# Kernel tuning notes

Hardware: AMD Instinct MI355X
Metric: run time of the kernel (lower is better)

## Reference

```python
import jax, jax.numpy as jnp
import numpy as np

P2 = 8
BN_EPS = 1e-5


def _slice_maps(p2):
    # Faithfully reproduce the buggy fs[:, i*j-1] indexing: later loop
    # iterations overwrite earlier ones; slots never written stay zero.
    last = {}
    for i in range(1, p2 + 1):
        for j in range(1, p2 + 1):
            last[i * j - 1] = (i - 1, j - 1)
    src_i = np.zeros(p2 * p2, np.int32)
    src_j = np.zeros(p2 * p2, np.int32)
    mask = np.zeros(p2 * p2, np.float32)
    for k, (ii, jj) in last.items():
        src_i[k], src_j[k], mask[k] = ii, jj, 1.0
    # unslice: output patch (i,j) reads slot (i+1)*(j+1)-1
    uns = np.array([[(i + 1) * (j + 1) - 1 for j in range(p2)] for i in range(p2)], np.int32)
    return src_i, src_j, mask, uns


def setup_inputs() -> dict:
    key = jax.random.key(0)
    ks = jax.random.split(key, 16)
    C, N, p2 = 32, 8, P2
    s = 0.05
    inp = {
        "x": jax.random.normal(ks[0], (8, C, 512, 512), jnp.float32),
        "w30": jax.random.normal(ks[1], (N, C, 3, 3), jnp.float32) * s,
        "b30": jnp.zeros((N,), jnp.float32),
        "w10": jax.random.normal(ks[2], (C, C), jnp.float32) * s,
        "b10": jnp.zeros((C,), jnp.float32),
        "w11": jax.random.normal(ks[3], (N, N), jnp.float32) * s,
        "b11": jnp.zeros((N,), jnp.float32),
        "w12a": jax.random.normal(ks[4], (p2, p2 * p2), jnp.float32) * s,
        "b12a": jnp.zeros((p2,), jnp.float32),
        "w12b": jax.random.normal(ks[5], (p2, p2), jnp.float32) * s,
        "b12b": jnp.zeros((p2,), jnp.float32),
        "w12c": jax.random.normal(ks[6], (p2 * p2, p2), jnp.float32) * s,
        "b12c": jnp.zeros((p2 * p2,), jnp.float32),
        "w31": jax.random.normal(ks[7], (C, C), jnp.float32) * s,
        "b31": jnp.zeros((C,), jnp.float32),
        "bn_gamma": jnp.ones((C,), jnp.float32),
        "bn_beta": jnp.zeros((C,), jnp.float32),
        "bn_mean": jnp.zeros((C,), jnp.float32),
        "bn_var": jnp.ones((C,), jnp.float32),
    }
    return inp


def reference(x, w30, b30, w10, b10, w11, b11, w12a, b12a, w12b, b12b,
              w12c, b12c, w31, b31, bn_gamma, bn_beta, bn_mean, bn_var):
    p2 = P2
    b, C, H, W = x.shape
    h, wd = H // p2, W // p2
    L = h * wd
    N = w30.shape[0]
    src_i, src_j, mask_np, uns = _slice_maps(p2)

    # --- slice into patches (with the original's overwrite/zero semantics) ---
    patches = x.reshape(b, C, p2, h, p2, wd).transpose(0, 2, 4, 1, 3, 5)  # [b,p2,p2,C,h,w]
    fs = patches[:, src_i, src_j] * jnp.asarray(mask_np)[None, :, None, None, None]
    fs = fs.reshape(b * p2 * p2, C, h, wd)

    # --- graph_convolution ---
    B = jax.lax.conv_general_dilated(fs, w30, (1, 1), 'SAME',
            dimension_numbers=('NCHW', 'OIHW', 'NCHW')) + b30[None, :, None, None]
    B = jax.nn.relu(B)                                    # [bp, N, h, w]
    B1 = B.reshape(b * p2 * p2, N, L)
    fs1 = fs.reshape(b * p2 * p2, C, L)
    fs2 = jnp.einsum('bnl,bcl->bnc', B1, fs1)              # [bp, N, C]
    fs3 = jax.nn.relu(jnp.einsum('on,bnc->boc', w11, fs2) + b11[None, :, None])
    fs5 = jax.nn.relu(jnp.einsum('oc,bcn->bon', w10, fs3.transpose(0, 2, 1)) + b10[None, :, None])  # [bp,C,N]
    fs6 = jnp.einsum('bnl,bcn->bcl', B1, fs5)              # [bp, C, L]
    fs6 = fs6.reshape(b, p2 * p2, C, h, wd)

    fg = x.reshape(b, C, 8, H // 8, 8, W // 8).mean(axis=(3, 5))  # [b,C,8,8]
    fg1 = fg.reshape(b, C, p2 * p2).transpose(0, 2, 1)            # [b, p2^2, C]
    g = jax.nn.relu(jnp.einsum('ok,bkc->boc', w12a, fg1) + b12a[None, :, None])
    g = jax.nn.relu(jnp.einsum('ok,bkc->boc', w12b, g) + b12b[None, :, None])
    g = jax.nn.sigmoid(jnp.einsum('ok,bkc->boc', w12c, g) + b12c[None, :, None])  # [b,p2^2,C]
    out5 = g[:, :, :, None, None] * fs6                            # [b,p2^2,C,h,w]

    # --- unslice back to image (patch (i,j) reads slot (i+1)*(j+1)-1) ---
    gathered = out5[:, uns]                                        # [b,p2,p2,C,h,w]
    out = gathered.transpose(0, 3, 1, 4, 2, 5).reshape(b, C, H, W)

    # --- conv31: 1x1 conv + BatchNorm(eval) + ReLU, residual add ---
    y = jnp.einsum('oc,bchw->bohw', w31, out) + b31[None, :, None, None]
    y = (y - bn_mean[None, :, None, None]) * jax.lax.rsqrt(bn_var[None, :, None, None] + BN_EPS)
    y = jax.nn.relu(y * bn_gamma[None, :, None, None] + bn_beta[None, :, None, None])
    return y + x
```

## Files before the change

kernel.cpp:

```cpp
#include <hip/hip_runtime.h>
#include <math.h>
#include <stdint.h>

#define HW 512
#define NACT 30

struct Maps {
    int src_i[64];
    int src_j[64];
    int mask[64];
    int aidx[64];
    int act_k[NACT];
};

static Maps make_maps() {
    Maps m;
    for (int k = 0; k < 64; k++) { m.src_i[k]=0; m.src_j[k]=0; m.mask[k]=0; m.aidx[k]=-1; }
    for (int i = 1; i <= 8; i++)
        for (int j = 1; j <= 8; j++) {
            int k = i*j-1;
            m.src_i[k]=i-1; m.src_j[k]=j-1; m.mask[k]=1;
        }
    int cnt=0;
    for (int k=0;k<64;k++) if (m.mask[k]) { m.aidx[k]=cnt; if (cnt < NACT) m.act_k[cnt]=k; cnt++; }
    return m;
}

__global__ __launch_bounds__(256) void k_zero(float* __restrict__ p, int n) {
    int i = blockIdx.x*256 + threadIdx.x;
    if (i < n) p[i] = 0.f;
}

__global__ __launch_bounds__(256) void k_fg(const float* __restrict__ x, float* __restrict__ fgw) {
    int blk = blockIdx.x;
    int k = blk & 63;
    int bc = blk >> 6;
    int c = bc & 31;
    int b = bc >> 5;
    int pi = k >> 3, pj = k & 7;
    const float* xp = x + (size_t)(b*32+c)*HW*HW;
    int t = threadIdx.x;
    float s = 0.f;
    #pragma unroll
    for (int ii = 0; ii < 4; ii++) {
        int idx4 = t + 256*ii;
        int y = idx4 >> 4;
        int xx = (idx4 & 15) * 4;
        float4 v = *(const float4*)(xp + (size_t)(pi*64 + y)*HW + pj*64 + xx);
        s += v.x + v.y + v.z + v.w;
    }
    for (int off = 32; off > 0; off >>= 1) s += __shfl_down(s, off);
    __shared__ float p[4];
    if ((t & 63) == 0) p[t >> 6] = s;
    __syncthreads();
    if (t == 0) {
        float tot = p[0]+p[1]+p[2]+p[3];
        fgw[(b*64 + k)*32 + c] = tot * (1.0f/4096.0f);
    }
}

__global__ void k_g(const float* __restrict__ fgw,
                    const float* __restrict__ w12a, const float* __restrict__ b12a,
                    const float* __restrict__ w12b, const float* __restrict__ b12b,
                    const float* __restrict__ w12c, const float* __restrict__ b12c,
                    float* __restrict__ g) {
    int b = blockIdx.x;
    int c = threadIdx.x;
    if (c >= 32) return;
    float fg[64];
    #pragma unroll
    for (int k = 0; k < 64; k++) fg[k] = fgw[(b*64+k)*32 + c];
    float g1[8], g2[8];
    #pragma unroll
    for (int o = 0; o < 8; o++) {
        float v = b12a[o];
        #pragma unroll
        for (int k2 = 0; k2 < 64; k2++) v += w12a[o*64+k2]*fg[k2];
        g1[o] = fmaxf(v, 0.f);
    }
    #pragma unroll
    for (int o = 0; o < 8; o++) {
        float v = b12b[o];
        #pragma unroll
        for (int k2 = 0; k2 < 8; k2++) v += w12b[o*8+k2]*g1[k2];
        g2[o] = fmaxf(v, 0.f);
    }
    for (int o = 0; o < 64; o++) {
        float v = b12c[o];
        #pragma unroll
        for (int k2 = 0; k2 < 8; k2++) v += w12c[o*8+k2]*g2[k2];
        g[(b*64+o)*32 + c] = 1.f / (1.f + expf(-v));
    }
}

__global__ __launch_bounds__(256) void k_conv(
        const float* __restrict__ x, const float* __restrict__ w30,
        const float* __restrict__ b30, float* __restrict__ B, Maps m) {
    int blk = blockIdx.x;
    int rt = blockIdx.y;
    int a = blk % NACT, b = blk / NACT;
    int k = m.act_k[a];
    int spi = m.src_i[k], spj = m.src_j[k];
    int r0 = rt*8;

    __shared__ float wlc[576];
    __shared__ __align__(16) float xs[8*10*72];

    int t = threadIdx.x;
    for (int idx = t; idx < 8*10*72; idx += 256) xs[idx] = 0.f;

    int col = t & 63, tl = t >> 6;
    float acc[2][8];
    #pragma unroll
    for (int rr=0; rr<2; rr++)
        #pragma unroll
        for (int n=0;n<8;n++) acc[rr][n]=0.f;

    const float* xb = x + (size_t)b*32*HW*HW;

    for (int c0 = 0; c0 < 32; c0 += 8) {
        __syncthreads();
        for (int idx = t; idx < 576; idx += 256) {
            int cc = idx / 72;
            int rem = idx - cc*72;
            int dydx = rem >> 3;
            int n = rem & 7;
            wlc[idx] = w30[(n*32 + c0 + cc)*9 + dydx];
        }
        #pragma unroll
        for (int it = 0; it < 5; it++) {
            int idx = t + 256*it;
            int cc = idx / 160;
            int rem = idx - cc*160;
            int r = rem >> 4;
            int q = rem & 15;
            int pr = r0 - 1 + r;
            float4 v = make_float4(0.f,0.f,0.f,0.f);
            if (pr >= 0 && pr < 64)
                v = *(const float4*)(xb + (size_t)(c0+cc)*HW*HW + (size_t)(spi*64+pr)*HW + spj*64 + q*4);
            *(float4*)(xs + cc*720 + r*72 + 4 + q*4) = v;
        }
        __syncthreads();
        for (int cc = 0; cc < 8; cc++) {
            const float* xrow = xs + cc*720 + (tl*2)*72 + 3 + col;
            float xv[4][3];
            #pragma unroll
            for (int r4 = 0; r4 < 4; r4++)
                #pragma unroll
                for (int d = 0; d < 3; d++)
                    xv[r4][d] = xrow[r4*72 + d];
            const float* wb = wlc + cc*72;
            #pragma unroll
            for (int dy = 0; dy < 3; dy++) {
                #pragma unroll
                for (int dx = 0; dx < 3; dx++) {
                    float4 wa0 = *(const float4*)(wb + (dy*3+dx)*8);
                    float4 wa1 = *(const float4*)(wb + (dy*3+dx)*8 + 4);
                    #pragma unroll
                    for (int rr = 0; rr < 2; rr++) {
                        float xvv = xv[rr+dy][dx];
                        acc[rr][0] = fmaf(xvv, wa0.x, acc[rr][0]);
                        acc[rr][1] = fmaf(xvv, wa0.y, acc[rr][1]);
                        acc[rr][2] = fmaf(xvv, wa0.z, acc[rr][2]);
                        acc[rr][3] = fmaf(xvv, wa0.w, acc[rr][3]);
                        acc[rr][4] = fmaf(xvv, wa1.x, acc[rr][4]);
                        acc[rr][5] = fmaf(xvv, wa1.y, acc[rr][5]);
                        acc[rr][6] = fmaf(xvv, wa1.z, acc[rr][6]);
                        acc[rr][7] = fmaf(xvv, wa1.w, acc[rr][7]);
                    }
                }
            }
        }
    }
    float* Bp = B + (size_t)(b*NACT+a)*8*4096;
    #pragma unroll
    for (int rr=0; rr<2; rr++) {
        int y = r0 + tl*2 + rr;
        #pragma unroll
        for (int n=0;n<8;n++)
            Bp[n*4096 + y*64 + col] = fmaxf(acc[rr][n] + b30[n], 0.f);
    }
}

__global__ __launch_bounds__(256) void k_fs2a(
        const float* __restrict__ x, const float* __restrict__ B,
        float* __restrict__ fs2g, Maps m) {
    int blk = blockIdx.x;
    int rt = blockIdx.y;
    int a = blk % NACT, b = blk / NACT;
    int k = m.act_k[a];
    int spi = m.src_i[k], spj = m.src_j[k];
    int l0 = rt*128;

    __shared__ __align__(16) float xs[32*132];

    int t = threadIdx.x;
    const float* xb = x + (size_t)b*32*HW*HW;
    #pragma unroll
    for (int q4 = 0; q4 < 4; q4++) {
        int idx = t + 256*q4;
        int c = idx >> 5, lq = idx & 31;
        int l = l0 + lq*4;
        int y = l >> 6, xx = l & 63;
        float4 v = *(const float4*)(xb + (size_t)c*HW*HW + (size_t)(spi*64+y)*HW + spj*64 + xx);
        *(float4*)(xs + c*132 + lq*4) = v;
    }
    __syncthreads();

    int n = t >> 5, c = t & 31;
    const float4* Bg4 = (const float4*)(B + (size_t)(b*NACT+a)*8*4096 + (size_t)n*4096 + l0);
    const float4* xs4 = (const float4*)(xs + c*132);
    float facc = 0.f;
    #pragma unroll 8
    for (int q = 0; q < 32; q++) {
        float4 bv = Bg4[q];
        float4 xv = xs4[q];
        facc = fmaf(bv.x, xv.x, facc);
        facc = fmaf(bv.y, xv.y, facc);
        facc = fmaf(bv.z, xv.z, facc);
        facc = fmaf(bv.w, xv.w, facc);
    }
    atomicAdd(&fs2g[(size_t)(b*NACT+a)*256 + n*32 + c], facc);
}

__global__ __launch_bounds__(256) void k_fs3(
        const float* __restrict__ fs2g,
        const float* __restrict__ w11, const float* __restrict__ b11,
        const float* __restrict__ w10, const float* __restrict__ b10,
        float* __restrict__ fs5, Maps m) {
    int blk = blockIdx.x;
    int a = blk % NACT, b = blk / NACT;
    int k = m.act_k[a];
    __shared__ float fs2s[8*33], fs3s[8*33];
    int t = threadIdx.x;
    {
        int n = t >> 5, c = t & 31;
        fs2s[n*33+c] = fs2g[(size_t)(b*NACT+a)*256 + n*32 + c];
    }
    __syncthreads();
    {
        int o = t >> 5, c = t & 31;
        float v = b11[o];
        #pragma unroll
        for (int n=0;n<8;n++) v += w11[o*8+n]*fs2s[n*33+c];
        fs3s[o*33+c] = fmaxf(v, 0.f);
    }
    __syncthreads();
    {
        int cp = t >> 3, n = t & 7;
        float v = b10[cp];
        #pragma unroll
        for (int c=0;c<32;c++) v += w10[cp*32+c]*fs3s[n*33+c];
        fs5[((size_t)(b*64+k)*32 + cp)*8 + n] = fmaxf(v, 0.f);
    }
}

__global__ __launch_bounds__(256) void k_out(
        const float* __restrict__ x, const float* __restrict__ B,
        const float* __restrict__ fs5, const float* __restrict__ g,
        const float* __restrict__ w31, const float* __restrict__ b31,
        const float* __restrict__ gamma, const float* __restrict__ beta,
        const float* __restrict__ mean, const float* __restrict__ var,
        float* __restrict__ out, Maps m) {
    int blk = blockIdx.x;
    int rt = blockIdx.y;
    int ij = blk & 63, b = blk >> 6;
    int i = ij >> 3, j = ij & 7;
    int K = (i+1)*(j+1) - 1;
    int aK = m.aidx[K];
    __shared__ float Ms[256];
    __shared__ float ss2[32], sh2[32];
    int t = threadIdx.x;
    {
        int o = t >> 3, n = t & 7;
        const float* f5 = fs5 + (size_t)(b*64+K)*32*8;
        const float* gg = g + (size_t)(b*64+K)*32;
        float v = 0.f;
        #pragma unroll
        for (int c=0;c<32;c++) v += w31[o*32+c]*gg[c]*f5[c*8+n];
        Ms[o*8+n] = v;
    }
    if (t < 32) {
        float sc = rsqrtf(var[t] + 1e-5f) * gamma[t];
        ss2[t] = sc;
        sh2[t] = (b31[t] - mean[t])*sc + beta[t];
    }
    __syncthreads();

    int r = t >> 4, q = t & 15;
    int y = rt*16 + r;
    int Y = i*64 + y;
    int X = j*64 + q*4;
    const float* Bp = B + (size_t)(b*NACT+aK)*8*4096 + y*64 + q*4;
    const float* xb = x + (size_t)b*32*HW*HW + (size_t)Y*HW + X;
    float* ob = out + (size_t)b*32*HW*HW + (size_t)Y*HW + X;

    float4 Bv[8];
    #pragma unroll
    for (int n=0;n<8;n++) Bv[n] = *(const float4*)(Bp + n*4096);

    #pragma unroll 4
    for (int o = 0; o < 32; o++) {
        float4 Ma = *(const float4*)(Ms + o*8);
        float4 Mb = *(const float4*)(Ms + o*8 + 4);
        float so = ss2[o], ho = sh2[o];
        float4 xv = *(const float4*)(xb + (size_t)o*HW*HW);
        float4 yv;
        yv.x = Bv[0].x*Ma.x + Bv[1].x*Ma.y + Bv[2].x*Ma.z + Bv[3].x*Ma.w
             + Bv[4].x*Mb.x + Bv[5].x*Mb.y + Bv[6].x*Mb.z + Bv[7].x*Mb.w;
        yv.y = Bv[0].y*Ma.x + Bv[1].y*Ma.y + Bv[2].y*Ma.z + Bv[3].y*Ma.w
             + Bv[4].y*Mb.x + Bv[5].y*Mb.y + Bv[6].y*Mb.z + Bv[7].y*Mb.w;
        yv.z = Bv[0].z*Ma.x + Bv[1].z*Ma.y + Bv[2].z*Ma.z + Bv[3].z*Ma.w
             + Bv[4].z*Mb.x + Bv[5].z*Mb.y + Bv[6].z*Mb.z + Bv[7].z*Mb.w;
        yv.w = Bv[0].w*Ma.x + Bv[1].w*Ma.y + Bv[2].w*Ma.z + Bv[3].w*Ma.w
             + Bv[4].w*Mb.x + Bv[5].w*Mb.y + Bv[6].w*Mb.z + Bv[7].w*Mb.w;
        float4 res;
        res.x = fmaxf(yv.x*so + ho, 0.f) + xv.x;
        res.y = fmaxf(yv.y*so + ho, 0.f) + xv.y;
        res.z = fmaxf(yv.z*so + ho, 0.f) + xv.z;
        res.w = fmaxf(yv.w*so + ho, 0.f) + xv.w;
        *(float4*)(ob + (size_t)o*HW*HW) = res;
    }
}

extern "C" void kernel_launch(void* const* d_in, const int* in_sizes, int n_in,
                              void* d_out, int out_size, void* d_ws, size_t ws_size,
                              hipStream_t stream) {
    const float* x    = (const float*)d_in[0];
    const float* w30  = (const float*)d_in[1];
    const float* b30  = (const float*)d_in[2];
    const float* w10  = (const float*)d_in[3];
    const float* b10  = (const float*)d_in[4];
    const float* w11  = (const float*)d_in[5];
    const float* b11  = (const float*)d_in[6];
    const float* w12a = (const float*)d_in[7];
    const float* b12a = (const float*)d_in[8];
    const float* w12b = (const float*)d_in[9];
    const float* b12b = (const float*)d_in[10];
    const float* w12c = (const float*)d_in[11];
    const float* b12c = (const float*)d_in[12];
    const float* w31  = (const float*)d_in[13];
    const float* b31  = (const float*)d_in[14];
    const float* gam  = (const float*)d_in[15];
    const float* bet  = (const float*)d_in[16];
    const float* mea  = (const float*)d_in[17];
    const float* var  = (const float*)d_in[18];
    float* out = (float*)d_out;

    float* ws   = (float*)d_ws;
    float* B    = ws;
    float* fs5  = B + 7864320;
    float* fgw  = fs5 + 131072;
    float* g    = fgw + 16384;
    float* fs2g = g + 16384;

    static Maps m = make_maps();

    k_zero<<<dim3(240),     256, 0, stream>>>(fs2g, 61440);
    k_fg  <<<dim3(16384),   256, 0, stream>>>(x, fgw);
    k_g   <<<dim3(8),        64, 0, stream>>>(fgw, w12a, b12a, w12b, b12b, w12c, b12c, g);
    k_conv<<<dim3(240, 8),  256, 0, stream>>>(x, w30, b30, B, m);
    k_fs2a<<<dim3(240, 32), 256, 0, stream>>>(x, B, fs2g, m);
    k_fs3 <<<dim3(240),     256, 0, stream>>>(fs2g, w11, b11, w10, b10, fs5, m);
    k_out <<<dim3(512, 4),  256, 0, stream>>>(x, B, fs5, g, w31, b31, gam, bet, mea, var, out, m);
}
```

Measured before the change: 730.9 us.

## Fuse patch mean pooling into conv kernel and drop shared-memory staging

The 3x3 conv kernel now loads all 32 channels' weights once, reads input rows directly from global memory, and gets horizontal neighbours through wave shuffles, so the shared-memory tiles of x are gone. While it reads the active patches, it also sums them for the adaptive average pool and adds the partial sums into fgw with atomics. k_fg now only covers the 34 inactive patches, which avoids re-reading those regions of x. The zeroing kernel is extended to cover both fgw and fs2g. The cost is atomic adds, extra shuffles, and uncoalesced scalar global loads in the conv.

```diff
diff --git a/kernel.cpp b/kernel.cpp
--- a/kernel.cpp
+++ b/kernel.cpp
@@ -4,6 +4,7 @@
 
 #define HW 512
 #define NACT 30
+#define NINACT 34
 
 struct Maps {
     int src_i[64];
@@ -11,6 +12,7 @@
     int mask[64];
     int aidx[64];
     int act_k[NACT];
+    int inact_k[NINACT];
 };
 
 static Maps make_maps() {
@@ -21,8 +23,11 @@
             int k = i*j-1;
             m.src_i[k]=i-1; m.src_j[k]=j-1; m.mask[k]=1;
         }
-    int cnt=0;
-    for (int k=0;k<64;k++) if (m.mask[k]) { m.aidx[k]=cnt; if (cnt < NACT) m.act_k[cnt]=k; cnt++; }
+    int cnt=0, icnt=0;
+    for (int k=0;k<64;k++) {
+        if (m.mask[k]) { m.aidx[k]=cnt; if (cnt < NACT) m.act_k[cnt]=k; cnt++; }
+        else           { if (icnt < NINACT) m.inact_k[icnt]=k; icnt++; }
+    }
     return m;
 }
 
@@ -31,12 +36,13 @@
     if (i < n) p[i] = 0.f;
 }
 
-__global__ __launch_bounds__(256) void k_fg(const float* __restrict__ x, float* __restrict__ fgw) {
-    int blk = blockIdx.x;
-    int k = blk & 63;
-    int bc = blk >> 6;
+__global__ __launch_bounds__(256) void k_fg(const float* __restrict__ x, float* __restrict__ fgw, Maps m) {
+    int blk = blockIdx.x;
+    int q = blk % NINACT;
+    int bc = blk / NINACT;
     int c = bc & 31;
     int b = bc >> 5;
+    int k = m.inact_k[q];
     int pi = k >> 3, pj = k & 7;
     const float* xp = x + (size_t)(b*32+c)*HW*HW;
     int t = threadIdx.x;
@@ -95,7 +101,8 @@
 
 __global__ __launch_bounds__(256) void k_conv(
         const float* __restrict__ x, const float* __restrict__ w30,
-        const float* __restrict__ b30, float* __restrict__ B, Maps m) {
+        const float* __restrict__ b30, float* __restrict__ B,
+        float* __restrict__ fgw, Maps m) {
     int blk = blockIdx.x;
     int rt = blockIdx.y;
     int a = blk % NACT, b = blk / NACT;
@@ -103,82 +110,92 @@
     int spi = m.src_i[k], spj = m.src_j[k];
     int r0 = rt*8;
 
-    __shared__ float wlc[576];
-    __shared__ __align__(16) float xs[8*10*72];
-
-    int t = threadIdx.x;
-    for (int idx = t; idx < 8*10*72; idx += 256) xs[idx] = 0.f;
-
-    int col = t & 63, tl = t >> 6;
+    __shared__ float wl[2304];
+    __shared__ float fg_part[128];
+
+    int t = threadIdx.x;
+    for (int idx = t; idx < 2304; idx += 256) {
+        int c = idx / 72;
+        int rem = idx - c*72;
+        int dydx = rem >> 3;
+        int n = rem & 7;
+        wl[idx] = w30[(n*32 + c)*9 + dydx];
+    }
+    if (t < 128) fg_part[t] = 0.f;
+
+    int col = t & 63, w = t >> 6;
     float acc[2][8];
     #pragma unroll
     for (int rr=0; rr<2; rr++)
         #pragma unroll
         for (int n=0;n<8;n++) acc[rr][n]=0.f;
 
-    const float* xb = x + (size_t)b*32*HW*HW;
-
-    for (int c0 = 0; c0 < 32; c0 += 8) {
-        __syncthreads();
-        for (int idx = t; idx < 576; idx += 256) {
-            int cc = idx / 72;
-            int rem = idx - cc*72;
-            int dydx = rem >> 3;
-            int n = rem & 7;
-            wlc[idx] = w30[(n*32 + c0 + cc)*9 + dydx];
+    const float* xb = x + (size_t)b*32*HW*HW + (size_t)(spi*64)*HW + spj*64 + col;
+    int prbase = r0 + w*2 - 1;
+    __syncthreads();
+
+    #pragma unroll 2
+    for (int cc = 0; cc < 32; cc++) {
+        const float* xp = xb + (size_t)cc*HW*HW;
+        float rv[4];
+        #pragma unroll
+        for (int ri=0; ri<4; ri++) {
+            int pr = prbase + ri;
+            rv[ri] = (pr >= 0 && pr < 64) ? xp[(size_t)pr*HW] : 0.f;
         }
-        #pragma unroll
-        for (int it = 0; it < 5; it++) {
-            int idx = t + 256*it;
-            int cc = idx / 160;
-            int rem = idx - cc*160;
-            int r = rem >> 4;
-            int q = rem & 15;
-            int pr = r0 - 1 + r;
-            float4 v = make_float4(0.f,0.f,0.f,0.f);
-            if (pr >= 0 && pr < 64)
-                v = *(const float4*)(xb + (size_t)(c0+cc)*HW*HW + (size_t)(spi*64+pr)*HW + spj*64 + q*4);
-            *(float4*)(xs + cc*720 + r*72 + 4 + q*4) = v;
+        float lv[4], hv[4];
+        #pragma unroll
+        for (int ri=0; ri<4; ri++) {
+            float xl = __shfl_up(rv[ri], 1);
+            float xh = __shfl_down(rv[ri], 1);
+            lv[ri] = (col == 0)  ? 0.f : xl;
+            hv[ri] = (col == 63) ? 0.f : xh;
         }
-        __syncthreads();
-        for (int cc = 0; cc < 8; cc++) {
-            const float* xrow = xs + cc*720 + (tl*2)*72 + 3 + col;
-            float xv[4][3];
+        const float* wb = wl + cc*72;
+        #pragma unroll
+        for (int dy = 0; dy < 3; dy++) {
             #pragma unroll
-            for (int r4 = 0; r4 < 4; r4++)
-                #pragma unroll
-                for (int d = 0; d < 3; d++)
-                    xv[r4][d] = xrow[r4*72 + d];
-            const float* wb = wlc + cc*72;
-            #pragma unroll
-            for (int dy = 0; dy < 3; dy++) {
-                #pragma unroll
-                for (int dx = 0; dx < 3; dx++) {
-                    float4 wa0 = *(const float4*)(wb + (dy*3+dx)*8);
-                    float4 wa1 = *(const float4*)(wb + (dy*3+dx)*8 + 4);
-                    #pragma unroll
-                    for (int rr = 0; rr < 2; rr++) {
-                        float xvv = xv[rr+dy][dx];
-                        acc[rr][0] = fmaf(xvv, wa0.x, acc[rr][0]);
-                        acc[rr][1] = fmaf(xvv, wa0.y, acc[rr][1]);
-                        acc[rr][2] = fmaf(xvv, wa0.z, acc[rr][2]);
-                        acc[rr][3] = fmaf(xvv, wa0.w, acc[rr][3]);
-                        acc[rr][4] = fmaf(xvv, wa1.x, acc[rr][4]);
-                        acc[rr][5] = fmaf(xvv, wa1.y, acc[rr][5]);
-                        acc[rr][6] = fmaf(xvv, wa1.z, acc[rr][6]);
-                        acc[rr][7] = fmaf(xvv, wa1.w, acc[rr][7]);
-                    }
-                }
+            for (int dx = 0; dx < 3; dx++) {
+                float4 wa0 = *(const float4*)(wb + (dy*3+dx)*8);
+                float4 wa1 = *(const float4*)(wb + (dy*3+dx)*8 + 4);
+                float x0 = (dx==0) ? lv[dy]   : ((dx==1) ? rv[dy]   : hv[dy]);
+                float x1 = (dx==0) ? lv[dy+1] : ((dx==1) ? rv[dy+1] : hv[dy+1]);
+                acc[0][0] = fmaf(x0, wa0.x, acc[0][0]);
+                acc[0][1] = fmaf(x0, wa0.y, acc[0][1]);
+                acc[0][2] = fmaf(x0, wa0.z, acc[0][2]);
+                acc[0][3] = fmaf(x0, wa0.w, acc[0][3]);
+                acc[0][4] = fmaf(x0, wa1.x, acc[0][4]);
+                acc[0][5] = fmaf(x0, wa1.y, acc[0][5]);
+                acc[0][6] = fmaf(x0, wa1.z, acc[0][6]);
+                acc[0][7] = fmaf(x0, wa1.w, acc[0][7]);
+                acc[1][0] = fmaf(x1, wa0.x, acc[1][0]);
+                acc[1][1] = fmaf(x1, wa0.y, acc[1][1]);
+                acc[1][2] = fmaf(x1, wa0.z, acc[1][2]);
+                acc[1][3] = fmaf(x1, wa0.w, acc[1][3]);
+                acc[1][4] = fmaf(x1, wa1.x, acc[1][4]);
+                acc[1][5] = fmaf(x1, wa1.y, acc[1][5]);
+                acc[1][6] = fmaf(x1, wa1.z, acc[1][6]);
+                acc[1][7] = fmaf(x1, wa1.w, acc[1][7]);
             }
         }
-    }
+        float s = rv[1] + rv[2];
+        #pragma unroll
+        for (int off = 1; off < 64; off <<= 1) s += __shfl_xor(s, off);
+        if (col == 0) fg_part[w*32 + cc] += s;
+    }
+
     float* Bp = B + (size_t)(b*NACT+a)*8*4096;
     #pragma unroll
     for (int rr=0; rr<2; rr++) {
-        int y = r0 + tl*2 + rr;
+        int y = r0 + w*2 + rr;
         #pragma unroll
         for (int n=0;n<8;n++)
             Bp[n*4096 + y*64 + col] = fmaxf(acc[rr][n] + b30[n], 0.f);
+    }
+    __syncthreads();
+    if (t < 32) {
+        float v = fg_part[t] + fg_part[32+t] + fg_part[64+t] + fg_part[96+t];
+        atomicAdd(&fgw[(b*64 + k)*32 + t], v * (1.0f/4096.0f));
     }
 }
 
@@ -356,10 +373,10 @@
 
     static Maps m = make_maps();
 
-    k_zero<<<dim3(240),     256, 0, stream>>>(fs2g, 61440);
-    k_fg  <<<dim3(16384),   256, 0, stream>>>(x, fgw);
+    k_zero<<<dim3(368),     256, 0, stream>>>(fgw, 94208);
+    k_conv<<<dim3(240, 8),  256, 0, stream>>>(x, w30, b30, B, fgw, m);
+    k_fg  <<<dim3(8704),    256, 0, stream>>>(x, fgw, m);
     k_g   <<<dim3(8),        64, 0, stream>>>(fgw, w12a, b12a, w12b, b12b, w12c, b12c, g);
-    k_conv<<<dim3(240, 8),  256, 0, stream>>>(x, w30, b30, B, m);
     k_fs2a<<<dim3(240, 32), 256, 0, stream>>>(x, B, fs2g, m);
     k_fs3 <<<dim3(240),     256, 0, stream>>>(fs2g, w11, b11, w10, b10, fs5, m);
     k_out <<<dim3(512, 4),  256, 0, stream>>>(x, B, fs5, g, w31, b31, gam, bet, mea, var, out, m);
```

Measured after the change: 762.0 us. 4.3% more time.

## Fuse patch-mean pooling for active patches into fs2a, pool only inactive patches

Applied to the files above, without the earlier changes.

The fs2a kernel already stages each active patch tile of x in shared memory, so it now also sums those tiles per channel and atomically adds the scaled result into the pooled-feature buffer. The standalone pooling kernel then only handles the 34 patches that are never sliced, which cuts its reads of x roughly in half. The zeroing kernel is widened to clear the pooled buffer as well, and launch order changes so pooling runs after fs2a. This costs extra atomics and a short serial per-channel reduction by 32 threads in each fs2a block.

```diff
diff --git a/kernel.cpp b/kernel.cpp
--- a/kernel.cpp
+++ b/kernel.cpp
@@ -4,6 +4,7 @@
 
 #define HW 512
 #define NACT 30
+#define NINACT 34
 
 struct Maps {
     int src_i[64];
@@ -11,6 +12,7 @@
     int mask[64];
     int aidx[64];
     int act_k[NACT];
+    int inact_k[NINACT];
 };
 
 static Maps make_maps() {
@@ -21,8 +23,11 @@
             int k = i*j-1;
             m.src_i[k]=i-1; m.src_j[k]=j-1; m.mask[k]=1;
         }
-    int cnt=0;
-    for (int k=0;k<64;k++) if (m.mask[k]) { m.aidx[k]=cnt; if (cnt < NACT) m.act_k[cnt]=k; cnt++; }
+    int cnt=0, icnt=0;
+    for (int k=0;k<64;k++) {
+        if (m.mask[k]) { m.aidx[k]=cnt; if (cnt < NACT) m.act_k[cnt]=k; cnt++; }
+        else           { if (icnt < NINACT) m.inact_k[icnt]=k; icnt++; }
+    }
     return m;
 }
 
@@ -31,12 +36,13 @@
     if (i < n) p[i] = 0.f;
 }
 
-__global__ __launch_bounds__(256) void k_fg(const float* __restrict__ x, float* __restrict__ fgw) {
-    int blk = blockIdx.x;
-    int k = blk & 63;
-    int bc = blk >> 6;
+__global__ __launch_bounds__(256) void k_fg(const float* __restrict__ x, float* __restrict__ fgw, Maps m) {
+    int blk = blockIdx.x;
+    int q = blk % NINACT;
+    int bc = blk / NINACT;
     int c = bc & 31;
     int b = bc >> 5;
+    int k = m.inact_k[q];
     int pi = k >> 3, pj = k & 7;
     const float* xp = x + (size_t)(b*32+c)*HW*HW;
     int t = threadIdx.x;
@@ -184,7 +190,7 @@
 
 __global__ __launch_bounds__(256) void k_fs2a(
         const float* __restrict__ x, const float* __restrict__ B,
-        float* __restrict__ fs2g, Maps m) {
+        float* __restrict__ fs2g, float* __restrict__ fgw, Maps m) {
     int blk = blockIdx.x;
     int rt = blockIdx.y;
     int a = blk % NACT, b = blk / NACT;
@@ -221,6 +227,17 @@
         facc = fmaf(bv.w, xv.w, facc);
     }
     atomicAdd(&fs2g[(size_t)(b*NACT+a)*256 + n*32 + c], facc);
+
+    if (t < 32) {
+        const float4* xc4 = (const float4*)(xs + t*132);
+        float s = 0.f;
+        #pragma unroll 8
+        for (int q = 0; q < 32; q++) {
+            float4 v = xc4[q];
+            s += v.x + v.y + v.z + v.w;
+        }
+        atomicAdd(&fgw[(b*64 + k)*32 + t], s * (1.0f/4096.0f));
+    }
 }
 
 __global__ __launch_bounds__(256) void k_fs3(
@@ -356,11 +373,11 @@
 
     static Maps m = make_maps();
 
-    k_zero<<<dim3(240),     256, 0, stream>>>(fs2g, 61440);
-    k_fg  <<<dim3(16384),   256, 0, stream>>>(x, fgw);
+    k_zero<<<dim3(368),     256, 0, stream>>>(fgw, 94208);
+    k_conv<<<dim3(240, 8),  256, 0, stream>>>(x, w30, b30, B, m);
+    k_fs2a<<<dim3(240, 32), 256, 0, stream>>>(x, B, fs2g, fgw, m);
+    k_fg  <<<dim3(8704),    256, 0, stream>>>(x, fgw, m);
     k_g   <<<dim3(8),        64, 0, stream>>>(fgw, w12a, b12a, w12b, b12b, w12c, b12c, g);
-    k_conv<<<dim3(240, 8),  256, 0, stream>>>(x, w30, b30, B, m);
-    k_fs2a<<<dim3(240, 32), 256, 0, stream>>>(x, B, fs2g, m);
     k_fs3 <<<dim3(240),     256, 0, stream>>>(fs2g, w11, b11, w10, b10, fs5, m);
     k_out <<<dim3(512, 4),  256, 0, stream>>>(x, B, fs5, g, w31, b31, gam, bet, mea, var, out, m);
 }
```

Result: faster. 675.8 us (-7.5%).
